# Performance work log

Hardware: AMD Instinct MI355X
Metric: run time of the kernel (lower is better)

## Reference

```python
import jax, jax.numpy as jnp
import numpy as np

INPUT_DIM = 768
STATE_DIM = 128
LN_EPS = 1e-5
CLAMP = 10.0


def setup_inputs() -> dict:
    key = jax.random.key(0)
    ks = jax.random.split(key, 9)
    B, T, D, S = 128, 256, INPUT_DIM, STATE_DIM
    x = jax.random.normal(ks[0], (B, T, D), dtype=jnp.float32)
    A = jax.random.normal(ks[1], (S, S), dtype=jnp.float32) * 0.01
    # nn.Linear weights are [out_features, in_features]
    B_w = jax.random.normal(ks[2], (S, D), dtype=jnp.float32) * (1.0 / np.sqrt(D))
    C_w = jax.random.normal(ks[3], (D, S), dtype=jnp.float32) * (1.0 / np.sqrt(S))
    D_w = jax.random.normal(ks[4], (D, D), dtype=jnp.float32) * (1.0 / np.sqrt(D))
    gate_w = jax.random.normal(ks[5], (2, D), dtype=jnp.float32) * (1.0 / np.sqrt(D))
    gate_b = jnp.zeros((2,), dtype=jnp.float32)
    ln_gamma = jnp.ones((D,), dtype=jnp.float32)
    ln_beta = jnp.zeros((D,), dtype=jnp.float32)
    return {"x": x, "A": A, "B_w": B_w, "C_w": C_w, "D_w": D_w,
            "gate_w": gate_w, "gate_b": gate_b,
            "ln_gamma": ln_gamma, "ln_beta": ln_beta}


def reference(x, A, B_w, C_w, D_w, gate_w, gate_b, ln_gamma, ln_beta):
    B, T, D = x.shape
    S = A.shape[0]
    residual = x
    # Precompute input projection for all timesteps: [B, T, S]
    Bx = jnp.einsum('btd,sd->bts', x, B_w)

    def step(state, bx_t):
        # state: [B, S]; state @ A.T + B(x_t), clamped
        state = jnp.clip(state @ A.T + bx_t, -CLAMP, CLAMP)
        return state, state

    init = jnp.zeros((B, S), dtype=x.dtype)
    _, states = jax.lax.scan(step, init, jnp.swapaxes(Bx, 0, 1))  # [T, B, S]
    states = jnp.swapaxes(states, 0, 1)  # [B, T, S]

    # Output projection (vectorized over all timesteps)
    out = jnp.einsum('bts,ds->btd', states, C_w) + jnp.einsum('btd,ed->bte', x, D_w)

    # Gating mix with residual
    gate = jax.nn.softmax(jnp.einsum('btd,gd->btg', x, gate_w) + gate_b, axis=-1)
    out = gate[..., 0:1] * out + gate[..., 1:2] * residual

    # LayerNorm (dropout is identity in eval)
    mu = jnp.mean(out, axis=-1, keepdims=True)
    var = jnp.var(out, axis=-1, keepdims=True)
    out = (out - mu) * jax.lax.rsqrt(var + LN_EPS) * ln_gamma + ln_beta
    return out
```

## Files before the change

### kernel.cpp

```cpp
#include <hip/hip_runtime.h>
#include <hip/hip_bf16.h>
#include <stdint.h>

typedef __bf16 bf16;
typedef __bf16 bf16x4 __attribute__((ext_vector_type(4)));
typedef __bf16 bf16x8 __attribute__((ext_vector_type(8)));
typedef float  f32x4  __attribute__((ext_vector_type(4)));

static constexpr int BB = 128;
static constexpr int TT = 256;
static constexpr int DD = 768;
static constexpr int SS = 128;
static constexpr int MM = BB * TT;
static constexpr int KW1 = DD + SS;

__device__ __forceinline__ void gload16(const void* g, void* l) {
  __builtin_amdgcn_global_load_lds(
      (const __attribute__((address_space(1))) void*)(uintptr_t)g,
      (__attribute__((address_space(3))) void*)(uintptr_t)l, 16, 0, 0);
}

__global__ __launch_bounds__(256) void k0_convert(
    const float* __restrict__ B_w, const float* __restrict__ D_w,
    const float* __restrict__ C_w, bf16* __restrict__ W0, bf16* __restrict__ W1) {
  int i = blockIdx.x * 256 + threadIdx.x;
  if (i < SS * DD) {
    W0[i] = (bf16)B_w[i];
  } else {
    int j = i - SS * DD;
    int n = j / KW1;
    int k = j - n * KW1;
    float v = (k < DD) ? D_w[n * DD + k] : C_w[n * SS + (k - DD)];
    W1[j] = (bf16)v;
  }
}

__global__ __launch_bounds__(256) void k0x_convert(
    const float* __restrict__ x, bf16* __restrict__ xb) {
  int i = blockIdx.x * 256 + threadIdx.x;
  const float4* src = (const float4*)x;
  float4 a = src[i * 2], b = src[i * 2 + 1];
  bf16x8 h;
  h[0] = (bf16)a.x; h[1] = (bf16)a.y; h[2] = (bf16)a.z; h[3] = (bf16)a.w;
  h[4] = (bf16)b.x; h[5] = (bf16)b.y; h[6] = (bf16)b.z; h[7] = (bf16)b.w;
  *(bf16x8*)&xb[i * 8] = h;
}

template <int TAG>
__global__ __launch_bounds__(256) void kg(
    const bf16* __restrict__ A1, const bf16* __restrict__ A2,
    const bf16* __restrict__ W, void* __restrict__ Cv,
    int kt1, int kt2, int lda1, int lda2, int ldb, int ldc, int mode) {
  __shared__ __align__(16) bf16 As[128 * 64];
  __shared__ __align__(16) bf16 Bs[128 * 64];

  const int tid = threadIdx.x;
  const int lane = tid & 63;
  const int wv = tid >> 6;
  const int wr = wv >> 1, wc = wv & 1;
  const int lr = lane & 15, lh = lane >> 4;
  const int bn0 = blockIdx.x * 128;
  const int bm0 = blockIdx.y * 128;

  const int l_row = lane >> 3;
  const int l_col = (lane & 7) * 8;

  f32x4 acc[4][4] = {};
  const int KT = kt1 + kt2;

  for (int kt = 0; kt < KT; ++kt) {
    __syncthreads();
    {
      const bf16* Ab; int lda;
      if (kt < kt1) { Ab = A1 + (size_t)bm0 * lda1 + kt * 64; lda = lda1; }
      else          { Ab = A2 + (size_t)bm0 * lda2 + (kt - kt1) * 64; lda = lda2; }
      #pragma unroll
      for (int it = 0; it < 4; ++it) {
        int c = wv * 4 + it;
        gload16(Ab + (size_t)(c * 8 + l_row) * lda + l_col, &As[c * 512]);
      }
    }
    {
      const bf16* Bb = W + (size_t)bn0 * ldb + kt * 64;
      #pragma unroll
      for (int it = 0; it < 4; ++it) {
        int c = wv * 4 + it;
        gload16(Bb + (size_t)(c * 8 + l_row) * ldb + l_col, &Bs[c * 512]);
      }
    }
    __syncthreads();
    #pragma unroll
    for (int kk = 0; kk < 2; ++kk) {
      bf16x8 af[4], bfr[4];
      #pragma unroll
      for (int f = 0; f < 4; ++f)
        af[f] = *(const bf16x8*)&As[(wr * 64 + f * 16 + lr) * 64 + kk * 32 + lh * 8];
      #pragma unroll
      for (int f = 0; f < 4; ++f)
        bfr[f] = *(const bf16x8*)&Bs[(wc * 64 + f * 16 + lr) * 64 + kk * 32 + lh * 8];
      #pragma unroll
      for (int fi = 0; fi < 4; ++fi)
        #pragma unroll
        for (int fj = 0; fj < 4; ++fj)
          acc[fi][fj] = __builtin_amdgcn_mfma_f32_16x16x32_bf16(
              af[fi], bfr[fj], acc[fi][fj], 0, 0, 0);
    }
  }
  #pragma unroll
  for (int fi = 0; fi < 4; ++fi)
    #pragma unroll
    for (int fj = 0; fj < 4; ++fj) {
      int row = bm0 + wr * 64 + fi * 16 + lh * 4;
      int col = bn0 + wc * 64 + fj * 16 + lr;
      if (mode == 0) {
        float* Cp = (float*)Cv + (size_t)row * ldc + col;
        #pragma unroll
        for (int r = 0; r < 4; ++r) Cp[(size_t)r * ldc] = acc[fi][fj][r];
      } else if (mode == 1) {
        bf16* Cp = (bf16*)Cv + (size_t)row * ldc + col;
        #pragma unroll
        for (int r = 0; r < 4; ++r) Cp[(size_t)r * ldc] = (bf16)acc[fi][fj][r];
      } else {
        float* Cp = (float*)Cv + (size_t)row * ldc + col;
        #pragma unroll
        for (int r = 0; r < 4; ++r) Cp[(size_t)r * ldc] += acc[fi][fj][r];
      }
    }
}

__global__ __launch_bounds__(256) void k_fused(
    const bf16* __restrict__ xb, const bf16* __restrict__ W1,
    float* __restrict__ out, bf16* SB, const float* __restrict__ A) {
  __shared__ __align__(16) char sraw[34304];

  if (blockIdx.x < 128) {
    float* st   = (float*)sraw;
    float* part = (float*)(sraw + 1024);
    float* bxb  = (float*)(sraw + 1536);

    const int tid = threadIdx.x;
    const int s = tid & 127;
    const int q = tid >> 7;
    bf16* Bxb = SB + (size_t)blockIdx.x * TT * SS;

    float areg[64];
    {
      const float* Ar = A + s * SS + q * 64;
      #pragma unroll
      for (int j = 0; j < 16; ++j) {
        float4 v = *(const float4*)(Ar + j * 4);
        areg[j * 4 + 0] = v.x; areg[j * 4 + 1] = v.y;
        areg[j * 4 + 2] = v.z; areg[j * 4 + 3] = v.w;
      }
    }
    if (tid < SS) st[tid] = 0.f;

    {
      bf16x8 c0 = *(const bf16x8*)(Bxb + tid * 16);
      bf16x8 c1 = *(const bf16x8*)(Bxb + tid * 16 + 8);
      float* d0 = &bxb[tid * 16];
      #pragma unroll
      for (int e = 0; e < 8; ++e) d0[e] = (float)c0[e];
      #pragma unroll
      for (int e = 0; e < 8; ++e) d0[8 + e] = (float)c1[e];
    }
    bf16x8 n0 = *(const bf16x8*)(Bxb + 4096 + tid * 16);
    bf16x8 n1 = *(const bf16x8*)(Bxb + 4096 + tid * 16 + 8);
    __syncthreads();

    int p = 0, cur = 0;
    for (int ch = 0; ch < 8; ++ch) {
      #pragma unroll 1
      for (int t2 = 0; t2 < 32; ++t2) {
        const float* stp = st + p * SS;
        float a0 = 0.f, a1 = 0.f, a2 = 0.f, a3 = 0.f;
        #pragma unroll
        for (int j = 0; j < 64; j += 4) {
          float4 sv = *(const float4*)(stp + (q << 6) + j);
          a0 += areg[j]     * sv.x;
          a1 += areg[j + 1] * sv.y;
          a2 += areg[j + 2] * sv.z;
          a3 += areg[j + 3] * sv.w;
        }
        float partial = (a0 + a1) + (a2 + a3);
        if (q) part[s] = partial;
        __syncthreads();
        if (!q) {
          float tot = partial + part[s] + bxb[cur * 4096 + t2 * SS + s];
          tot = fminf(10.f, fmaxf(-10.f, tot));
          st[(p ^ 1) * SS + s] = tot;
          Bxb[(size_t)(ch * 32 + t2) * SS + s] = (bf16)tot;
        }
        __syncthreads();
        p ^= 1;
      }
      if (ch < 7) {
        float* dn = &bxb[(cur ^ 1) * 4096 + tid * 16];
        #pragma unroll
        for (int e = 0; e < 8; ++e) dn[e] = (float)n0[e];
        #pragma unroll
        for (int e = 0; e < 8; ++e) dn[8 + e] = (float)n1[e];
        if (ch < 6) {
          n0 = *(const bf16x8*)(Bxb + (ch + 2) * 4096 + tid * 16);
          n1 = *(const bf16x8*)(Bxb + (ch + 2) * 4096 + tid * 16 + 8);
        }
        __syncthreads();
        cur ^= 1;
      }
    }
  } else {
    bf16* As = (bf16*)sraw;
    bf16* Bs = (bf16*)(sraw + 16384);

    const int gb = blockIdx.x - 128;
    const int bn0 = (gb % 6) * 128;
    const int bm0 = (gb / 6) * 128;

    const int tid = threadIdx.x;
    const int lane = tid & 63;
    const int wv = tid >> 6;
    const int wr = wv >> 1, wc = wv & 1;
    const int lr = lane & 15, lh = lane >> 4;
    const int l_row = lane >> 3;
    const int l_col = (lane & 7) * 8;

    f32x4 acc[4][4] = {};

    for (int kt = 0; kt < 12; ++kt) {
      __syncthreads();
      {
        const bf16* Ab = xb + (size_t)bm0 * DD + kt * 64;
        #pragma unroll
        for (int it = 0; it < 4; ++it) {
          int c = wv * 4 + it;
          gload16(Ab + (size_t)(c * 8 + l_row) * DD + l_col, &As[c * 512]);
        }
      }
      {
        const bf16* Bb = W1 + (size_t)bn0 * KW1 + kt * 64;
        #pragma unroll
        for (int it = 0; it < 4; ++it) {
          int c = wv * 4 + it;
          gload16(Bb + (size_t)(c * 8 + l_row) * KW1 + l_col, &Bs[c * 512]);
        }
      }
      __syncthreads();
      #pragma unroll
      for (int kk = 0; kk < 2; ++kk) {
        bf16x8 af[4], bfr[4];
        #pragma unroll
        for (int f = 0; f < 4; ++f)
          af[f] = *(const bf16x8*)&As[(wr * 64 + f * 16 + lr) * 64 + kk * 32 + lh * 8];
        #pragma unroll
        for (int f = 0; f < 4; ++f)
          bfr[f] = *(const bf16x8*)&Bs[(wc * 64 + f * 16 + lr) * 64 + kk * 32 + lh * 8];
        #pragma unroll
        for (int fi = 0; fi < 4; ++fi)
          #pragma unroll
          for (int fj = 0; fj < 4; ++fj)
            acc[fi][fj] = __builtin_amdgcn_mfma_f32_16x16x32_bf16(
                af[fi], bfr[fj], acc[fi][fj], 0, 0, 0);
      }
    }
    #pragma unroll
    for (int fi = 0; fi < 4; ++fi)
      #pragma unroll
      for (int fj = 0; fj < 4; ++fj) {
        int row = bm0 + wr * 64 + fi * 16 + lh * 4;
        int col = bn0 + wc * 64 + fj * 16 + lr;
        float* Cp = out + (size_t)row * DD + col;
        #pragma unroll
        for (int r = 0; r < 4; ++r) Cp[(size_t)r * DD] = acc[fi][fj][r];
      }
  }
}

__global__ __launch_bounds__(256) void k_gemm(
    const float* __restrict__ A1, const bf16* __restrict__ A2,
    const bf16* __restrict__ W, float* __restrict__ C,
    int kt1, int kt2, int lda1, int lda2, int ldb, int ldc) {
  __shared__ __align__(16) bf16 As[128][72];
  __shared__ __align__(16) bf16 Bs[128][72];

  const int tid = threadIdx.x;
  const int lane = tid & 63;
  const int wv = tid >> 6;
  const int wr = wv >> 1, wc = wv & 1;
  const int lr = lane & 15, lh = lane >> 4;
  const int bn0 = blockIdx.x * 128;
  const int bm0 = blockIdx.y * 128;

  f32x4 acc[4][4] = {};
  const int KT = kt1 + kt2;

  for (int kt = 0; kt < KT; ++kt) {
    __syncthreads();
    if (kt < kt1) {
      const float* Ab = A1 + (size_t)bm0 * lda1 + kt * 64;
      #pragma unroll
      for (int it = 0; it < 8; ++it) {
        int c = it * 256 + tid;
        int row = c >> 4, col = (c & 15) << 2;
        float4 v = *(const float4*)(Ab + (size_t)row * lda1 + col);
        bf16x4 h;
        h[0] = (bf16)v.x; h[1] = (bf16)v.y; h[2] = (bf16)v.z; h[3] = (bf16)v.w;
        *(bf16x4*)&As[row][col] = h;
      }
    } else {
      const bf16* Ab = A2 + (size_t)bm0 * lda2 + (kt - kt1) * 64;
      #pragma unroll
      for (int it = 0; it < 8; ++it) {
        int c = it * 256 + tid;
        int row = c >> 4, col = (c & 15) << 2;
        bf16x4 v = *(const bf16x4*)(Ab + (size_t)row * lda2 + col);
        *(bf16x4*)&As[row][col] = v;
      }
    }
    {
      const bf16* Bb = W + (size_t)bn0 * ldb + kt * 64;
      #pragma unroll
      for (int it = 0; it < 8; ++it) {
        int c = it * 256 + tid;
        int row = c >> 4, col = (c & 15) << 2;
        bf16x4 v = *(const bf16x4*)(Bb + (size_t)row * ldb + col);
        *(bf16x4*)&Bs[row][col] = v;
      }
    }
    __syncthreads();
    #pragma unroll
    for (int kk = 0; kk < 2; ++kk) {
      bf16x8 af[4], bfr[4];
      #pragma unroll
      for (int f = 0; f < 4; ++f)
        af[f] = *(const bf16x8*)&As[wr * 64 + f * 16 + lr][kk * 32 + lh * 8];
      #pragma unroll
      for (int f = 0; f < 4; ++f)
        bfr[f] = *(const bf16x8*)&Bs[wc * 64 + f * 16 + lr][kk * 32 + lh * 8];
      #pragma unroll
      for (int fi = 0; fi < 4; ++fi)
        #pragma unroll
        for (int fj = 0; fj < 4; ++fj)
          acc[fi][fj] = __builtin_amdgcn_mfma_f32_16x16x32_bf16(
              af[fi], bfr[fj], acc[fi][fj], 0, 0, 0);
    }
  }
  #pragma unroll
  for (int fi = 0; fi < 4; ++fi)
    #pragma unroll
    for (int fj = 0; fj < 4; ++fj) {
      int row = bm0 + wr * 64 + fi * 16 + lh * 4;
      int col = bn0 + wc * 64 + fj * 16 + lr;
      float* Cp = C + (size_t)row * ldc + col;
      #pragma unroll
      for (int r = 0; r < 4; ++r) Cp[(size_t)r * ldc] = acc[fi][fj][r];
    }
}

__global__ __launch_bounds__(512) void k2_scan(
    const float* __restrict__ Bx, const float* __restrict__ A,
    bf16* __restrict__ states) {
  __shared__ __align__(16) float st[2][SS];
  __shared__ __align__(16) float part[3][SS];
  __shared__ __align__(16) float bxb[2][32 * SS];

  const int tid = threadIdx.x;
  const int s = tid & 127;
  const int q = tid >> 7;
  const int b = blockIdx.x;

  float areg[32];
  {
    const float* Ar = A + s * SS + q * 32;
    #pragma unroll
    for (int j = 0; j < 8; ++j) {
      float4 v = *(const float4*)(Ar + j * 4);
      areg[j * 4 + 0] = v.x; areg[j * 4 + 1] = v.y;
      areg[j * 4 + 2] = v.z; areg[j * 4 + 3] = v.w;
    }
  }
  if (tid < SS) st[0][tid] = 0.f;

  const float* Bxb = Bx + (size_t)b * TT * SS;
  {
    float4 c0 = *(const float4*)(Bxb + tid * 4);
    float4 c1 = *(const float4*)(Bxb + 2048 + tid * 4);
    *(float4*)&bxb[0][tid * 4] = c0;
    *(float4*)&bxb[0][2048 + tid * 4] = c1;
  }
  float4 n0 = *(const float4*)(Bxb + 4096 + tid * 4);
  float4 n1 = *(const float4*)(Bxb + 4096 + 2048 + tid * 4);
  __syncthreads();

  bf16* so = states + (size_t)b * TT * SS;
  int p = 0, cur = 0;
  for (int ch = 0; ch < 8; ++ch) {
    #pragma unroll 1
    for (int t2 = 0; t2 < 32; ++t2) {
      const float* stp = st[p];
      float a0 = 0.f, a1 = 0.f, a2 = 0.f, a3 = 0.f;
      #pragma unroll
      for (int j = 0; j < 32; j += 4) {
        float4 sv = *(const float4*)(stp + (q << 5) + j);
        a0 += areg[j]     * sv.x;
        a1 += areg[j + 1] * sv.y;
        a2 += areg[j + 2] * sv.z;
        a3 += areg[j + 3] * sv.w;
      }
      float partial = (a0 + a1) + (a2 + a3);
      if (q) part[q - 1][s] = partial;
      __syncthreads();
      if (q == 0) {
        float tot = partial + part[0][s] + part[1][s] + part[2][s]
                  + bxb[cur][t2 * SS + s];
        tot = fminf(10.f, fmaxf(-10.f, tot));
        st[p ^ 1][s] = tot;
        so[(size_t)(ch * 32 + t2) * SS + s] = (bf16)tot;
      }
      __syncthreads();
      p ^= 1;
    }
    if (ch < 7) {
      *(float4*)&bxb[cur ^ 1][tid * 4] = n0;
      *(float4*)&bxb[cur ^ 1][2048 + tid * 4] = n1;
      if (ch < 6) {
        n0 = *(const float4*)(Bxb + (ch + 2) * 4096 + tid * 4);
        n1 = *(const float4*)(Bxb + (ch + 2) * 4096 + 2048 + tid * 4);
      }
      __syncthreads();
      cur ^= 1;
    }
  }
}

__global__ __launch_bounds__(256) void k4_epilogue(
    float* __restrict__ out, const float* __restrict__ x,
    const float* __restrict__ gate_w, const float* __restrict__ gate_b,
    const float* __restrict__ ln_g, const float* __restrict__ ln_b) {
  const int lane = threadIdx.x & 63;
  const int w = threadIdx.x >> 6;
  const int r = blockIdx.x * 4 + w;

  float4* orow = (float4*)(out + (size_t)r * DD);
  const float4* xrow = (const float4*)(x + (size_t)r * DD);
  const float4* g0w = (const float4*)gate_w;
  const float4* g1w = (const float4*)(gate_w + DD);

  float4 o[3], xv[3];
  float d = 0.f;
  #pragma unroll
  for (int i = 0; i < 3; ++i) {
    int c = i * 64 + lane;
    o[i] = orow[c];
    xv[i] = xrow[c];
    float4 w0 = g0w[c], w1 = g1w[c];
    d += xv[i].x * (w0.x - w1.x) + xv[i].y * (w0.y - w1.y)
       + xv[i].z * (w0.z - w1.z) + xv[i].w * (w0.w - w1.w);
  }
  #pragma unroll
  for (int off = 32; off > 0; off >>= 1) d += __shfl_xor(d, off);
  d += gate_b[0] - gate_b[1];
  float g0 = 1.f / (1.f + expf(-d));
  float g1 = 1.f - g0;

  float4 m[3];
  float s1 = 0.f, s2 = 0.f;
  #pragma unroll
  for (int i = 0; i < 3; ++i) {
    m[i].x = g0 * o[i].x + g1 * xv[i].x;
    m[i].y = g0 * o[i].y + g1 * xv[i].y;
    m[i].z = g0 * o[i].z + g1 * xv[i].z;
    m[i].w = g0 * o[i].w + g1 * xv[i].w;
    s1 += (m[i].x + m[i].y) + (m[i].z + m[i].w);
    s2 += (m[i].x * m[i].x + m[i].y * m[i].y)
        + (m[i].z * m[i].z + m[i].w * m[i].w);
  }
  #pragma unroll
  for (int off = 32; off > 0; off >>= 1) {
    s1 += __shfl_xor(s1, off);
    s2 += __shfl_xor(s2, off);
  }
  float mu = s1 * (1.f / 768.f);
  float var = s2 * (1.f / 768.f) - mu * mu;
  float rs = rsqrtf(var + 1e-5f);

  #pragma unroll
  for (int i = 0; i < 3; ++i) {
    int c = i * 64 + lane;
    float4 gg = ((const float4*)ln_g)[c];
    float4 bb = ((const float4*)ln_b)[c];
    float4 y;
    y.x = (m[i].x - mu) * rs * gg.x + bb.x;
    y.y = (m[i].y - mu) * rs * gg.y + bb.y;
    y.z = (m[i].z - mu) * rs * gg.z + bb.z;
    y.w = (m[i].w - mu) * rs * gg.w + bb.w;
    orow[c] = y;
  }
}

extern "C" void kernel_launch(void* const* d_in, const int* in_sizes, int n_in,
                              void* d_out, int out_size, void* d_ws, size_t ws_size,
                              hipStream_t stream) {
  const float* x   = (const float*)d_in[0];
  const float* A   = (const float*)d_in[1];
  const float* B_w = (const float*)d_in[2];
  const float* C_w = (const float*)d_in[3];
  const float* D_w = (const float*)d_in[4];
  const float* gw  = (const float*)d_in[5];
  const float* gb  = (const float*)d_in[6];
  const float* lng = (const float*)d_in[7];
  const float* lnb = (const float*)d_in[8];
  float* out = (float*)d_out;

  bf16* W0 = (bf16*)d_ws;
  bf16* W1 = W0 + SS * DD;
  bf16* SB = W1 + DD * KW1;
  bf16* xb = SB + (size_t)MM * SS;
  const size_t ws_need_fast =
      2ull * (SS * DD + DD * KW1 + (size_t)MM * SS + (size_t)MM * DD);
  const size_t ws_need_min = 2ull * (SS * DD + DD * KW1 + (size_t)MM * SS);

  k0_convert<<<dim3(3072), dim3(256), 0, stream>>>(B_w, D_w, C_w, W0, W1);

  if (ws_size >= ws_need_fast) {
    k0x_convert<<<dim3(12288), dim3(256), 0, stream>>>(x, xb);
    kg<1><<<dim3(1, 256), dim3(256), 0, stream>>>(
        xb, nullptr, W0, SB, 12, 0, DD, 0, DD, SS, 1);
    k_fused<<<dim3(128 + 1536), dim3(256), 0, stream>>>(xb, W1, out, SB, A);
    kg<3><<<dim3(6, 256), dim3(256), 0, stream>>>(
        SB, nullptr, W1 + DD, out, 2, 0, SS, 0, KW1, DD, 2);
  } else if (ws_size >= ws_need_min) {
    float* Bx = out + ((size_t)MM * DD - (size_t)MM * SS);
    bf16* states = SB;
    k_gemm<<<dim3(1, 256), dim3(256), 0, stream>>>(
        x, nullptr, W0, Bx, 12, 0, DD, 0, DD, SS);
    k2_scan<<<dim3(128), dim3(512), 0, stream>>>(Bx, A, states);
    k_gemm<<<dim3(6, 256), dim3(256), 0, stream>>>(
        x, states, W1, out, 12, 2, DD, SS, KW1, DD);
  }

  k4_epilogue<<<dim3(8192), dim3(256), 0, stream>>>(out, x, gw, gb, lng, lnb);
}
```

Before: 436.2 us.

## Fuse state projection, gating and LayerNorm into one tail kernel

```diff
diff --git a/kernel.cpp b/kernel.cpp
--- a/kernel.cpp
+++ b/kernel.cpp
@@ -35,15 +35,31 @@
   }
 }
 
-__global__ __launch_bounds__(256) void k0x_convert(
-    const float* __restrict__ x, bf16* __restrict__ xb) {
-  int i = blockIdx.x * 256 + threadIdx.x;
-  const float4* src = (const float4*)x;
-  float4 a = src[i * 2], b = src[i * 2 + 1];
-  bf16x8 h;
-  h[0] = (bf16)a.x; h[1] = (bf16)a.y; h[2] = (bf16)a.z; h[3] = (bf16)a.w;
-  h[4] = (bf16)b.x; h[5] = (bf16)b.y; h[6] = (bf16)b.z; h[7] = (bf16)b.w;
-  *(bf16x8*)&xb[i * 8] = h;
+__global__ __launch_bounds__(256) void k0x_gate(
+    const float* __restrict__ x, bf16* __restrict__ xb,
+    const float* __restrict__ gw, const float* __restrict__ gb,
+    float* __restrict__ glog) {
+  const int lane = threadIdx.x & 63;
+  const int wv = threadIdx.x >> 6;
+  const int r = blockIdx.x * 4 + wv;
+  const float4* xr = (const float4*)(x + (size_t)r * DD);
+  const float4* g0w = (const float4*)gw;
+  const float4* g1w = (const float4*)(gw + DD);
+  float d = 0.f;
+  #pragma unroll
+  for (int i = 0; i < 3; ++i) {
+    int c = i * 64 + lane;
+    float4 v = xr[c];
+    float4 w0 = g0w[c], w1 = g1w[c];
+    d += v.x * (w0.x - w1.x) + v.y * (w0.y - w1.y)
+       + v.z * (w0.z - w1.z) + v.w * (w0.w - w1.w);
+    bf16x4 h;
+    h[0] = (bf16)v.x; h[1] = (bf16)v.y; h[2] = (bf16)v.z; h[3] = (bf16)v.w;
+    *(bf16x4*)&xb[(size_t)r * DD + c * 4] = h;
+  }
+  #pragma unroll
+  for (int off = 32; off > 0; off >>= 1) d += __shfl_xor(d, off);
+  if (lane == 0) glog[r] = d + gb[0] - gb[1];
 }
 
 template <int TAG>
@@ -134,6 +150,7 @@
   __shared__ __align__(16) char sraw[34304];
 
   if (blockIdx.x < 128) {
+    __builtin_amdgcn_s_setprio(1);
     float* st   = (float*)sraw;
     float* part = (float*)(sraw + 1024);
     float* bxb  = (float*)(sraw + 1536);
@@ -275,6 +292,116 @@
   }
 }
 
+__global__ __launch_bounds__(256) void kT(
+    const bf16* __restrict__ SB, const bf16* __restrict__ Wc,
+    float* __restrict__ out, const float* __restrict__ x,
+    const float* __restrict__ glog, const float* __restrict__ ln_g,
+    const float* __restrict__ ln_b) {
+  __shared__ __align__(16) bf16 As[16 * 128];
+  __shared__ __align__(16) bf16 Ws[128 * 128];
+  __shared__ __align__(16) bf16 mbuf[16 * 768];
+  __shared__ float wpart[4][16][2];
+  __shared__ float mu_s[16], rs_s[16];
+
+  const int tid = threadIdx.x;
+  const int lane = tid & 63;
+  const int wv = tid >> 6;
+  const int lr = lane & 15, lh = lane >> 4;
+  const int m0 = blockIdx.x * 16;
+
+  {
+    const bf16* g = SB + (size_t)(m0 + wv * 4 + lh) * 128 + lr * 8;
+    gload16(g, &As[wv * 512]);
+  }
+
+  float g0v[4], g1v[4];
+  #pragma unroll
+  for (int r = 0; r < 4; ++r) {
+    float gl = glog[m0 + lh * 4 + r];
+    float g0 = 1.f / (1.f + expf(-gl));
+    g0v[r] = g0; g1v[r] = 1.f - g0;
+  }
+
+  float s1[4] = {0.f, 0.f, 0.f, 0.f}, s2[4] = {0.f, 0.f, 0.f, 0.f};
+
+  for (int st = 0; st < 6; ++st) {
+    const int n0 = st * 128;
+    __syncthreads();
+    #pragma unroll
+    for (int it = 0; it < 8; ++it) {
+      int c = wv * 8 + it;
+      const bf16* g = Wc + (size_t)(n0 + c * 4 + lh) * KW1 + lr * 8;
+      gload16(g, &Ws[c * 512]);
+    }
+    __syncthreads();
+    f32x4 acc0 = {0.f, 0.f, 0.f, 0.f}, acc1 = {0.f, 0.f, 0.f, 0.f};
+    #pragma unroll
+    for (int kk = 0; kk < 4; ++kk) {
+      bf16x8 af = *(const bf16x8*)&As[lr * 128 + kk * 32 + lh * 8];
+      bf16x8 b0 = *(const bf16x8*)&Ws[((wv * 2 + 0) * 16 + lr) * 128 + kk * 32 + lh * 8];
+      bf16x8 b1 = *(const bf16x8*)&Ws[((wv * 2 + 1) * 16 + lr) * 128 + kk * 32 + lh * 8];
+      acc0 = __builtin_amdgcn_mfma_f32_16x16x32_bf16(af, b0, acc0, 0, 0, 0);
+      acc1 = __builtin_amdgcn_mfma_f32_16x16x32_bf16(af, b1, acc1, 0, 0, 0);
+    }
+    #pragma unroll
+    for (int nn = 0; nn < 2; ++nn) {
+      const f32x4 av = nn ? acc1 : acc0;
+      int col = n0 + (wv * 2 + nn) * 16 + lr;
+      #pragma unroll
+      for (int r = 0; r < 4; ++r) {
+        int rowl = lh * 4 + r;
+        size_t gi = (size_t)(m0 + rowl) * DD + col;
+        float raw = av[r] + out[gi];
+        float mv = g0v[r] * raw + g1v[r] * x[gi];
+        s1[r] += mv; s2[r] += mv * mv;
+        mbuf[rowl * DD + col] = (bf16)mv;
+      }
+    }
+  }
+  #pragma unroll
+  for (int r = 0; r < 4; ++r) {
+    #pragma unroll
+    for (int off = 1; off < 16; off <<= 1) {
+      s1[r] += __shfl_xor(s1[r], off);
+      s2[r] += __shfl_xor(s2[r], off);
+    }
+  }
+  if (lr == 0) {
+    #pragma unroll
+    for (int r = 0; r < 4; ++r) {
+      wpart[wv][lh * 4 + r][0] = s1[r];
+      wpart[wv][lh * 4 + r][1] = s2[r];
+    }
+  }
+  __syncthreads();
+  if (tid < 16) {
+    float S1 = wpart[0][tid][0] + wpart[1][tid][0] + wpart[2][tid][0] + wpart[3][tid][0];
+    float S2 = wpart[0][tid][1] + wpart[1][tid][1] + wpart[2][tid][1] + wpart[3][tid][1];
+    float mu = S1 * (1.f / 768.f);
+    float var = S2 * (1.f / 768.f) - mu * mu;
+    mu_s[tid] = mu;
+    rs_s[tid] = rsqrtf(fmaxf(var, 0.f) + 1e-5f);
+  }
+  __syncthreads();
+  #pragma unroll
+  for (int i = 0; i < 12; ++i) {
+    int gq = i * 256 + tid;
+    int row = gq / 192;
+    int c4 = gq - row * 192;
+    int col = c4 * 4;
+    bf16x4 mv = *(const bf16x4*)&mbuf[row * DD + col];
+    float4 gg = *(const float4*)&ln_g[col];
+    float4 bb = *(const float4*)&ln_b[col];
+    float mu = mu_s[row], rs = rs_s[row];
+    float4 y;
+    y.x = ((float)mv[0] - mu) * rs * gg.x + bb.x;
+    y.y = ((float)mv[1] - mu) * rs * gg.y + bb.y;
+    y.z = ((float)mv[2] - mu) * rs * gg.z + bb.z;
+    y.w = ((float)mv[3] - mu) * rs * gg.w + bb.w;
+    *(float4*)&out[(size_t)(m0 + row) * DD + col] = y;
+  }
+}
+
 __global__ __launch_bounds__(256) void k_gemm(
     const float* __restrict__ A1, const bf16* __restrict__ A2,
     const bf16* __restrict__ W, float* __restrict__ C,
@@ -515,19 +642,21 @@
   bf16* W1 = W0 + SS * DD;
   bf16* SB = W1 + DD * KW1;
   bf16* xb = SB + (size_t)MM * SS;
-  const size_t ws_need_fast =
+  float* glog = (float*)(xb + (size_t)MM * DD);
+  const size_t base_bf16 =
       2ull * (SS * DD + DD * KW1 + (size_t)MM * SS + (size_t)MM * DD);
+  const size_t ws_need_full = base_bf16 + 4ull * MM;
   const size_t ws_need_min = 2ull * (SS * DD + DD * KW1 + (size_t)MM * SS);
 
   k0_convert<<<dim3(3072), dim3(256), 0, stream>>>(B_w, D_w, C_w, W0, W1);
 
-  if (ws_size >= ws_need_fast) {
-    k0x_convert<<<dim3(12288), dim3(256), 0, stream>>>(x, xb);
+  if (ws_size >= ws_need_full) {
+    k0x_gate<<<dim3(8192), dim3(256), 0, stream>>>(x, xb, gw, gb, glog);
     kg<1><<<dim3(1, 256), dim3(256), 0, stream>>>(
         xb, nullptr, W0, SB, 12, 0, DD, 0, DD, SS, 1);
     k_fused<<<dim3(128 + 1536), dim3(256), 0, stream>>>(xb, W1, out, SB, A);
-    kg<3><<<dim3(6, 256), dim3(256), 0, stream>>>(
-        SB, nullptr, W1 + DD, out, 2, 0, SS, 0, KW1, DD, 2);
+    kT<<<dim3(2048), dim3(256), 0, stream>>>(
+        SB, W1 + DD, out, x, glog, lng, lnb);
   } else if (ws_size >= ws_need_min) {
     float* Bx = out + ((size_t)MM * DD - (size_t)MM * SS);
     bf16* states = SB;
@@ -536,7 +665,6 @@
     k2_scan<<<dim3(128), dim3(512), 0, stream>>>(Bx, A, states);
     k_gemm<<<dim3(6, 256), dim3(256), 0, stream>>>(
         x, states, W1, out, 12, 2, DD, SS, KW1, DD);
-  }
-
-  k4_epilogue<<<dim3(8192), dim3(256), 0, stream>>>(out, x, gw, gb, lng, lnb);
-}
+    k4_epilogue<<<dim3(8192), dim3(256), 0, stream>>>(out, x, gw, gb, lng, lnb);
+  }
+}
```

New measurement: 411.3 us. 1.06x faster.
